# Optimization experiments

Hardware: AMD Instinct MI355X
Metric: run time of the kernel (lower is better)

The kernel has to match this reference:

```python
import jax, jax.numpy as jnp
import numpy as np


def _morpho(x, weight, bias, sign, padding, stride):
    # x: [B,C,H,W], weight: [B,C,kh,kw], bias: [B,C], sign: [B]
    B, C, H, W = x.shape
    kh, kw = weight.shape[-2:]
    # sign handling: if |sign| >= 1e-7 multiply by sign, else leave unchanged
    m = (jnp.abs(sign) >= 1e-7).astype(x.dtype)          # [B], constant (detached in torch)
    s = m * sign + (1.0 - m)                              # effective multiplier per sample
    xs = x * s[:, None, None, None]
    # unfold zero-pads, and sign*0 == 0, so padding signed x with zeros is equivalent
    xp = jnp.pad(xs, ((0, 0), (0, 0), (padding, padding), (padding, padding)))
    H2 = (H + 2 * padding - kh) // stride + 1
    W2 = (W + 2 * padding - kw) // stride + 1
    # direct windowed max-plus: y[b,c,i,j] = max_{p,q} xs_pad[b,c,i*s+p,j*s+q] + w[b,c,p,q]
    # small fixed kh*kw loop avoids materializing the B*C*kh*kw*L unfold tensor
    y = jnp.full((B, C, H2, W2), -jnp.inf, dtype=x.dtype)
    for p in range(kh):
        for q in range(kw):
            patch = jax.lax.slice(
                xp,
                (0, 0, p, q),
                (B, C, p + (H2 - 1) * stride + 1, q + (W2 - 1) * stride + 1),
                (1, 1, stride, stride),
            )  # [B,C,H2,W2]
            y = jnp.maximum(y, patch + weight[:, :, p, q][:, :, None, None])
    y = y + bias[:, :, None, None]
    return y * s[:, None, None, None]


def setup_inputs() -> dict:
    key = jax.random.key(0)
    k1, k2, k3, k4 = jax.random.split(key, 4)
    B, C, H, W, kh, kw = 16, 64, 128, 128, 5, 5
    return {
        "x": jax.random.normal(k1, (B, C, H, W), dtype=jnp.float32),
        "weight": jax.random.normal(k2, (B, C, kh, kw), dtype=jnp.float32) * 0.1,
        "bias": jax.random.normal(k3, (B, C), dtype=jnp.float32) * 0.1,
        "sign": jax.random.normal(k4, (B,), dtype=jnp.float32),
        "padding": 2,
        "stride": 1,
    }


def reference(x, weight, bias, sign, padding, stride):
    return _morpho(x, weight, bias, sign, padding, stride)
```

## Files before the change

### kernel.cpp

```cpp
#include <hip/hip_runtime.h>
#include <math.h>
#include <stdint.h>

#define HH 128
#define WW 128
#define LROWS 36
#define ROWU 72
#define UNITS 648
#define LDSU (LROWS * ROWU)

typedef __fp16 h2 __attribute__((ext_vector_type(2)));

__device__ __forceinline__ h2 h2max(h2 a, h2 b) { return __builtin_elementwise_max(a, b); }
__device__ __forceinline__ uint32_t h2u(h2 v) { return __builtin_bit_cast(uint32_t, v); }
__device__ __forceinline__ h2 uh2(uint32_t v) { return __builtin_bit_cast(h2, v); }

__global__ __launch_bounds__(256, 6) void morpho_kernel(
    const float* __restrict__ x,
    const float* __restrict__ wgt,
    const float* __restrict__ bias,
    const float* __restrict__ sign,
    float* __restrict__ out)
{
    __shared__ uint32_t lds[LDSU];

    const int blk  = blockIdx.x;
    const int quad = blk & 3;
    const int bc   = blk >> 2;
    const int b    = bc >> 6;

    const float* __restrict__ xp = x   + (size_t)bc * (HH * WW);
    float*       __restrict__ yp = out + (size_t)bc * (HH * WW);
    const float* __restrict__ wp = wgt + bc * 25;

    const float sgn = sign[b];
    const float s   = (fabsf(sgn) >= 1e-7f) ? sgn : 1.0f;
    const float bvs = bias[bc] * s;
    const __fp16 sh = (__fp16)s;
    const h2 s2 = { sh, sh };
    const h2 z2 = { (__fp16)0.f, (__fp16)0.f };

    const int t = threadIdx.x;

    float4 v0[3], v1[3];
    int urow[3], uuc[3];
    bool uin[3], uivalid[3];
#pragma unroll
    for (int k = 0; k < 3; ++k) {
        const int u   = t + k * 256;
        uin[k]        = (u < UNITS);
        const int row = u / 18;
        const int uc  = u - row * 18;
        urow[k] = row;  uuc[k] = uc;
        const int grow = quad * 32 - 2 + row;
        uivalid[k] = uin[k] && (uc >= 1) && (uc <= 16) && ((unsigned)grow < (unsigned)HH);
        const int rc = min(max(grow, 0), HH - 1);
        const int cc = min(max(uc * 8 - 8, 0), WW - 8);
        const float* gp = xp + rc * WW + cc;
        v0[k] = *reinterpret_cast<const float4*>(gp);
        v1[k] = *reinterpret_cast<const float4*>(gp + 4);
    }

    int ws[25];
#pragma unroll
    for (int k = 0; k < 25; ++k) {
        const __fp16 wh = (__fp16)wp[k];
        h2 wv2 = { wh, wh };
        ws[k] = __builtin_amdgcn_readfirstlane((int)h2u(wv2));
    }

#pragma unroll
    for (int k = 0; k < 3; ++k) {
        if (uin[k]) {
            const h2 m = uivalid[k] ? s2 : z2;
            const h2 h0 = __builtin_amdgcn_cvt_pkrtz(v0[k].x, v0[k].y) * m;
            const h2 h1 = __builtin_amdgcn_cvt_pkrtz(v0[k].z, v0[k].w) * m;
            const h2 hv = __builtin_amdgcn_cvt_pkrtz(v1[k].x, v1[k].y) * m;
            const h2 h3 = __builtin_amdgcn_cvt_pkrtz(v1[k].z, v1[k].w) * m;
            uint4 o;
            o.x = h2u(h0); o.y = h2u(h1); o.z = h2u(hv); o.w = h2u(h3);
            *reinterpret_cast<uint4*>(&lds[urow[k] * ROWU + uuc[k] * 4]) = o;
        }
    }

    __syncthreads();

    const int tx = t & 31;
    const int ty = t >> 5;
    h2 acc0[4], acc1[4];

#pragma unroll
    for (int r8 = 0; r8 < 8; ++r8) {
        const uint32_t* lp = &lds[(ty * 4 + r8) * ROWU + 2 * tx + 2];
        const uint32_t r1 = lp[1];
        const uint2   d23 = *reinterpret_cast<const uint2*>(lp + 2);
        const uint32_t r2 = d23.x, r3 = d23.y;
        const uint32_t r4 = lp[4];
        const uint32_t am1 = __builtin_amdgcn_alignbit(r2, r1, 16);
        const uint32_t a1  = __builtin_amdgcn_alignbit(r3, r2, 16);
        const uint32_t a3  = __builtin_amdgcn_alignbit(r4, r3, 16);
        const uint32_t P0a[5] = { r1, am1, r2, a1, r3 };
        const uint32_t P1a[5] = { r2, a1, r3, a3, r4 };

#pragma unroll
        for (int p = 0; p < 5; ++p) {
            const int oi = r8 - p;
            if (oi >= 0 && oi < 4) {
                {
                    const h2 t0 = uh2(P0a[0]) + uh2((uint32_t)ws[p * 5 + 0]);
                    const h2 t1 = uh2(P0a[1]) + uh2((uint32_t)ws[p * 5 + 1]);
                    const h2 t2 = uh2(P0a[2]) + uh2((uint32_t)ws[p * 5 + 2]);
                    const h2 t3 = uh2(P0a[3]) + uh2((uint32_t)ws[p * 5 + 3]);
                    const h2 t4 = uh2(P0a[4]) + uh2((uint32_t)ws[p * 5 + 4]);
                    h2 mm = h2max(h2max(h2max(t0, t1), h2max(t2, t3)), t4);
                    acc0[oi] = (p == 0) ? mm : h2max(acc0[oi], mm);
                }
                {
                    const h2 t0 = uh2(P1a[0]) + uh2((uint32_t)ws[p * 5 + 0]);
                    const h2 t1 = uh2(P1a[1]) + uh2((uint32_t)ws[p * 5 + 1]);
                    const h2 t2 = uh2(P1a[2]) + uh2((uint32_t)ws[p * 5 + 2]);
                    const h2 t3 = uh2(P1a[3]) + uh2((uint32_t)ws[p * 5 + 3]);
                    const h2 t4 = uh2(P1a[4]) + uh2((uint32_t)ws[p * 5 + 4]);
                    h2 mm = h2max(h2max(h2max(t0, t1), h2max(t2, t3)), t4);
                    acc1[oi] = (p == 0) ? mm : h2max(acc1[oi], mm);
                }
            }
        }
    }

    const int i0 = quad * 32 + ty * 4;
    const int j0 = tx * 4;
#pragma unroll
    for (int a = 0; a < 4; ++a) {
        float4 o;
        o.x = fmaf((float)acc0[a][0], s, bvs);
        o.y = fmaf((float)acc0[a][1], s, bvs);
        o.z = fmaf((float)acc1[a][0], s, bvs);
        o.w = fmaf((float)acc1[a][1], s, bvs);
        *reinterpret_cast<float4*>(yp + (size_t)(i0 + a) * WW + j0) = o;
    }
}

extern "C" void kernel_launch(void* const* d_in, const int* in_sizes, int n_in,
                              void* d_out, int out_size, void* d_ws, size_t ws_size,
                              hipStream_t stream) {
    (void)d_ws; (void)ws_size; (void)in_sizes; (void)n_in; (void)out_size;
    const float* x    = (const float*)d_in[0];
    const float* w    = (const float*)d_in[1];
    const float* bias = (const float*)d_in[2];
    const float* sign = (const float*)d_in[3];
    float* out = (float*)d_out;

    morpho_kernel<<<4096, 256, 0, stream>>>(x, w, bias, sign, out);
}
```

Before: 32.98 us.

## Replace LDS staging with direct global loads and fold sign into packed FMA

Drops the shared-memory tile and barrier. Each thread now loads its three float4 neighbours per input row straight from global memory and builds the shifted fp16 pairs in registers. The sign multiply moves from the staging step into a packed FMA with the weight. Block indices are remapped across the grid and launch bounds are raised to 8 waves per SIMD. This raises redundant global and L1/L2 traffic, since rows are reloaded by overlapping threads and blocks, in exchange for removing LDS writes and the sync and possibly raising occupancy.

```diff
diff --git a/kernel.cpp b/kernel.cpp
--- a/kernel.cpp
+++ b/kernel.cpp
@@ -4,10 +4,7 @@
 
 #define HH 128
 #define WW 128
-#define LROWS 36
-#define ROWU 72
-#define UNITS 648
-#define LDSU (LROWS * ROWU)
+#define NFLOATS (16 * 64 * HH * WW)
 
 typedef __fp16 h2 __attribute__((ext_vector_type(2)));
 
@@ -15,21 +12,25 @@
 __device__ __forceinline__ uint32_t h2u(h2 v) { return __builtin_bit_cast(uint32_t, v); }
 __device__ __forceinline__ h2 uh2(uint32_t v) { return __builtin_bit_cast(h2, v); }
 
-__global__ __launch_bounds__(256, 6) void morpho_kernel(
+#if __has_builtin(__builtin_elementwise_fma)
+#define H2FMA(a, b, c) __builtin_elementwise_fma((a), (b), (c))
+#else
+#define H2FMA(a, b, c) ((a) * (b) + (c))
+#endif
+
+__global__ __launch_bounds__(256, 8) void morpho_kernel(
     const float* __restrict__ x,
     const float* __restrict__ wgt,
     const float* __restrict__ bias,
     const float* __restrict__ sign,
     float* __restrict__ out)
 {
-    __shared__ uint32_t lds[LDSU];
-
-    const int blk  = blockIdx.x;
+    const int bid  = blockIdx.x;
+    const int blk  = (bid & 7) * 512 + (bid >> 3);
     const int quad = blk & 3;
     const int bc   = blk >> 2;
     const int b    = bc >> 6;
 
-    const float* __restrict__ xp = x   + (size_t)bc * (HH * WW);
     float*       __restrict__ yp = out + (size_t)bc * (HH * WW);
     const float* __restrict__ wp = wgt + bc * 25;
 
@@ -38,89 +39,78 @@
     const float bvs = bias[bc] * s;
     const __fp16 sh = (__fp16)s;
     const h2 s2 = { sh, sh };
-    const h2 z2 = { (__fp16)0.f, (__fp16)0.f };
 
-    const int t = threadIdx.x;
-
-    float4 v0[3], v1[3];
-    int urow[3], uuc[3];
-    bool uin[3], uivalid[3];
-#pragma unroll
-    for (int k = 0; k < 3; ++k) {
-        const int u   = t + k * 256;
-        uin[k]        = (u < UNITS);
-        const int row = u / 18;
-        const int uc  = u - row * 18;
-        urow[k] = row;  uuc[k] = uc;
-        const int grow = quad * 32 - 2 + row;
-        uivalid[k] = uin[k] && (uc >= 1) && (uc <= 16) && ((unsigned)grow < (unsigned)HH);
-        const int rc = min(max(grow, 0), HH - 1);
-        const int cc = min(max(uc * 8 - 8, 0), WW - 8);
-        const float* gp = xp + rc * WW + cc;
-        v0[k] = *reinterpret_cast<const float4*>(gp);
-        v1[k] = *reinterpret_cast<const float4*>(gp + 4);
-    }
-
-    int ws[25];
+    uint32_t wsu[25];
 #pragma unroll
     for (int k = 0; k < 25; ++k) {
         const __fp16 wh = (__fp16)wp[k];
-        h2 wv2 = { wh, wh };
-        ws[k] = __builtin_amdgcn_readfirstlane((int)h2u(wv2));
+        h2 w2 = { wh, wh };
+        wsu[k] = (uint32_t)__builtin_amdgcn_readfirstlane((int)h2u(w2));
     }
 
-#pragma unroll
-    for (int k = 0; k < 3; ++k) {
-        if (uin[k]) {
-            const h2 m = uivalid[k] ? s2 : z2;
-            const h2 h0 = __builtin_amdgcn_cvt_pkrtz(v0[k].x, v0[k].y) * m;
-            const h2 h1 = __builtin_amdgcn_cvt_pkrtz(v0[k].z, v0[k].w) * m;
-            const h2 hv = __builtin_amdgcn_cvt_pkrtz(v1[k].x, v1[k].y) * m;
-            const h2 h3 = __builtin_amdgcn_cvt_pkrtz(v1[k].z, v1[k].w) * m;
-            uint4 o;
-            o.x = h2u(h0); o.y = h2u(h1); o.z = h2u(hv); o.w = h2u(h3);
-            *reinterpret_cast<uint4*>(&lds[urow[k] * ROWU + uuc[k] * 4]) = o;
-        }
-    }
-
-    __syncthreads();
-
+    const int t  = threadIdx.x;
     const int tx = t & 31;
     const int ty = t >> 5;
+    const int j0 = tx * 4;
+    const int i0 = quad * 32 + ty * 4;
+    const int planeOff = bc * (HH * WW);
+
+    const bool mL = (tx > 0);
+    const bool mR = (tx < 31);
+
     h2 acc0[4], acc1[4];
 
 #pragma unroll
     for (int r8 = 0; r8 < 8; ++r8) {
-        const uint32_t* lp = &lds[(ty * 4 + r8) * ROWU + 2 * tx + 2];
-        const uint32_t r1 = lp[1];
-        const uint2   d23 = *reinterpret_cast<const uint2*>(lp + 2);
-        const uint32_t r2 = d23.x, r3 = d23.y;
-        const uint32_t r4 = lp[4];
-        const uint32_t am1 = __builtin_amdgcn_alignbit(r2, r1, 16);
-        const uint32_t a1  = __builtin_amdgcn_alignbit(r3, r2, 16);
-        const uint32_t a3  = __builtin_amdgcn_alignbit(r4, r3, 16);
-        const uint32_t P0a[5] = { r1, am1, r2, a1, r3 };
-        const uint32_t P1a[5] = { r2, a1, r3, a3, r4 };
+        const int  r  = i0 - 2 + r8;
+        const bool rv = ((unsigned)r < (unsigned)HH);
+        const int  rc = min(max(r, 0), HH - 1);
+        const int  oM = planeOff + rc * WW + j0;
+        const int  oL = max(oM - 4, 0);
+        const int  oR = min(oM + 4, NFLOATS - 4);
+        const float4 v0 = *reinterpret_cast<const float4*>(x + oL);
+        const float4 v1 = *reinterpret_cast<const float4*>(x + oM);
+        const float4 v2 = *reinterpret_cast<const float4*>(x + oR);
+
+        uint32_t e0 = h2u(__builtin_amdgcn_cvt_pkrtz(v0.z, v0.w));
+        uint32_t e1 = h2u(__builtin_amdgcn_cvt_pkrtz(v1.x, v1.y));
+        uint32_t e2 = h2u(__builtin_amdgcn_cvt_pkrtz(v1.z, v1.w));
+        uint32_t e3 = h2u(__builtin_amdgcn_cvt_pkrtz(v2.x, v2.y));
+        e0 = (rv && mL) ? e0 : 0u;
+        e1 = rv ? e1 : 0u;
+        e2 = rv ? e2 : 0u;
+        e3 = (rv && mR) ? e3 : 0u;
+        const uint32_t o0 = __builtin_amdgcn_alignbit(e1, e0, 16);
+        const uint32_t o1 = __builtin_amdgcn_alignbit(e2, e1, 16);
+        const uint32_t o2 = __builtin_amdgcn_alignbit(e3, e2, 16);
+
+        const uint32_t P0[5] = { e0, o0, e1, o1, e2 };
+        const uint32_t P1[5] = { e1, o1, e2, o2, e3 };
 
 #pragma unroll
         for (int p = 0; p < 5; ++p) {
             const int oi = r8 - p;
             if (oi >= 0 && oi < 4) {
+                const h2 w0 = uh2(wsu[p * 5 + 0]);
+                const h2 w1 = uh2(wsu[p * 5 + 1]);
+                const h2 w2 = uh2(wsu[p * 5 + 2]);
+                const h2 w3 = uh2(wsu[p * 5 + 3]);
+                const h2 w4 = uh2(wsu[p * 5 + 4]);
                 {
-                    const h2 t0 = uh2(P0a[0]) + uh2((uint32_t)ws[p * 5 + 0]);
-                    const h2 t1 = uh2(P0a[1]) + uh2((uint32_t)ws[p * 5 + 1]);
-                    const h2 t2 = uh2(P0a[2]) + uh2((uint32_t)ws[p * 5 + 2]);
-                    const h2 t3 = uh2(P0a[3]) + uh2((uint32_t)ws[p * 5 + 3]);
-                    const h2 t4 = uh2(P0a[4]) + uh2((uint32_t)ws[p * 5 + 4]);
+                    const h2 t0 = H2FMA(uh2(P0[0]), s2, w0);
+                    const h2 t1 = H2FMA(uh2(P0[1]), s2, w1);
+                    const h2 t2 = H2FMA(uh2(P0[2]), s2, w2);
+                    const h2 t3 = H2FMA(uh2(P0[3]), s2, w3);
+                    const h2 t4 = H2FMA(uh2(P0[4]), s2, w4);
                     h2 mm = h2max(h2max(h2max(t0, t1), h2max(t2, t3)), t4);
                     acc0[oi] = (p == 0) ? mm : h2max(acc0[oi], mm);
                 }
                 {
-                    const h2 t0 = uh2(P1a[0]) + uh2((uint32_t)ws[p * 5 + 0]);
-                    const h2 t1 = uh2(P1a[1]) + uh2((uint32_t)ws[p * 5 + 1]);
-                    const h2 t2 = uh2(P1a[2]) + uh2((uint32_t)ws[p * 5 + 2]);
-                    const h2 t3 = uh2(P1a[3]) + uh2((uint32_t)ws[p * 5 + 3]);
-                    const h2 t4 = uh2(P1a[4]) + uh2((uint32_t)ws[p * 5 + 4]);
+                    const h2 t0 = H2FMA(uh2(P1[0]), s2, w0);
+                    const h2 t1 = H2FMA(uh2(P1[1]), s2, w1);
+                    const h2 t2 = H2FMA(uh2(P1[2]), s2, w2);
+                    const h2 t3 = H2FMA(uh2(P1[3]), s2, w3);
+                    const h2 t4 = H2FMA(uh2(P1[4]), s2, w4);
                     h2 mm = h2max(h2max(h2max(t0, t1), h2max(t2, t3)), t4);
                     acc1[oi] = (p == 0) ? mm : h2max(acc1[oi], mm);
                 }
@@ -128,8 +118,6 @@
         }
     }
 
-    const int i0 = quad * 32 + ty * 4;
-    const int j0 = tx * 4;
 #pragma unroll
     for (int a = 0; a < 4; ++a) {
         float4 o;
```

Measured after the change: 33.54 us. No clear change (+1.7%).

## Process two row tiles per block with double-buffered LDS and up-front loads

Applied to the files above, without the earlier changes.

Each block now handles two 32-row tiles (half an image) instead of one. Global loads for both tiles are issued up front, and the second tile's conversion into a separate LDS buffer overlaps with the first tile's compute. The grid is halved and block IDs are remapped with an XCD-style swizzle. This amortizes the per-block weight setup and hides global latency, at the cost of doubled LDS and more registers, which can reduce occupancy under the existing launch bounds.

```diff
diff --git a/kernel.cpp b/kernel.cpp
--- a/kernel.cpp
+++ b/kernel.cpp
@@ -4,8 +4,8 @@
 
 #define HH 128
 #define WW 128
+#define ROWU 72
 #define LROWS 36
-#define ROWU 72
 #define UNITS 648
 #define LDSU (LROWS * ROWU)
 
@@ -22,11 +22,12 @@
     const float* __restrict__ sign,
     float* __restrict__ out)
 {
-    __shared__ uint32_t lds[LDSU];
+    __shared__ uint32_t lds[2][LDSU];
 
-    const int blk  = blockIdx.x;
-    const int quad = blk & 3;
-    const int bc   = blk >> 2;
+    const int bid  = blockIdx.x;
+    const int blk  = (bid & 7) * 256 + (bid >> 3);
+    const int half = blk & 1;
+    const int bc   = blk >> 1;
     const int b    = bc >> 6;
 
     const float* __restrict__ xp = x   + (size_t)bc * (HH * WW);
@@ -42,103 +43,125 @@
 
     const int t = threadIdx.x;
 
-    float4 v0[3], v1[3];
     int urow[3], uuc[3];
-    bool uin[3], uivalid[3];
+    bool uin[3];
 #pragma unroll
     for (int k = 0; k < 3; ++k) {
-        const int u   = t + k * 256;
-        uin[k]        = (u < UNITS);
-        const int row = u / 18;
-        const int uc  = u - row * 18;
-        urow[k] = row;  uuc[k] = uc;
-        const int grow = quad * 32 - 2 + row;
-        uivalid[k] = uin[k] && (uc >= 1) && (uc <= 16) && ((unsigned)grow < (unsigned)HH);
-        const int rc = min(max(grow, 0), HH - 1);
-        const int cc = min(max(uc * 8 - 8, 0), WW - 8);
-        const float* gp = xp + rc * WW + cc;
-        v0[k] = *reinterpret_cast<const float4*>(gp);
-        v1[k] = *reinterpret_cast<const float4*>(gp + 4);
+        const int u = t + k * 256;
+        uin[k] = (u < UNITS);
+        urow[k] = u / 18;
+        uuc[k]  = u - urow[k] * 18;
     }
 
-    int ws[25];
+    float4 vA0[3], vA1[3], vB0[3], vB1[3];
+#pragma unroll
+    for (int k = 0; k < 3; ++k) {
+        const int cc = min(max(uuc[k] * 8 - 8, 0), WW - 8);
+        {
+            const int grow = half * 64 - 2 + urow[k];
+            const int rc   = min(max(grow, 0), HH - 1);
+            const float* gp = xp + rc * WW + cc;
+            vA0[k] = *reinterpret_cast<const float4*>(gp);
+            vA1[k] = *reinterpret_cast<const float4*>(gp + 4);
+        }
+        {
+            const int grow = half * 64 + 30 + urow[k];
+            const int rc   = min(max(grow, 0), HH - 1);
+            const float* gp = xp + rc * WW + cc;
+            vB0[k] = *reinterpret_cast<const float4*>(gp);
+            vB1[k] = *reinterpret_cast<const float4*>(gp + 4);
+        }
+    }
+    asm volatile("" ::: "memory");
+
+    uint32_t wsu[25];
 #pragma unroll
     for (int k = 0; k < 25; ++k) {
         const __fp16 wh = (__fp16)wp[k];
-        h2 wv2 = { wh, wh };
-        ws[k] = __builtin_amdgcn_readfirstlane((int)h2u(wv2));
+        h2 w2 = { wh, wh };
+        wsu[k] = (uint32_t)__builtin_amdgcn_readfirstlane((int)h2u(w2));
     }
-
-#pragma unroll
-    for (int k = 0; k < 3; ++k) {
-        if (uin[k]) {
-            const h2 m = uivalid[k] ? s2 : z2;
-            const h2 h0 = __builtin_amdgcn_cvt_pkrtz(v0[k].x, v0[k].y) * m;
-            const h2 h1 = __builtin_amdgcn_cvt_pkrtz(v0[k].z, v0[k].w) * m;
-            const h2 hv = __builtin_amdgcn_cvt_pkrtz(v1[k].x, v1[k].y) * m;
-            const h2 h3 = __builtin_amdgcn_cvt_pkrtz(v1[k].z, v1[k].w) * m;
-            uint4 o;
-            o.x = h2u(h0); o.y = h2u(h1); o.z = h2u(hv); o.w = h2u(h3);
-            *reinterpret_cast<uint4*>(&lds[urow[k] * ROWU + uuc[k] * 4]) = o;
-        }
-    }
-
-    __syncthreads();
 
     const int tx = t & 31;
     const int ty = t >> 5;
-    h2 acc0[4], acc1[4];
+    const int j0 = tx * 4;
 
+    auto CVT_WRITE = [&](int buf, const float4* v0, const float4* v1, int tile) {
 #pragma unroll
-    for (int r8 = 0; r8 < 8; ++r8) {
-        const uint32_t* lp = &lds[(ty * 4 + r8) * ROWU + 2 * tx + 2];
-        const uint32_t r1 = lp[1];
-        const uint2   d23 = *reinterpret_cast<const uint2*>(lp + 2);
-        const uint32_t r2 = d23.x, r3 = d23.y;
-        const uint32_t r4 = lp[4];
-        const uint32_t am1 = __builtin_amdgcn_alignbit(r2, r1, 16);
-        const uint32_t a1  = __builtin_amdgcn_alignbit(r3, r2, 16);
-        const uint32_t a3  = __builtin_amdgcn_alignbit(r4, r3, 16);
-        const uint32_t P0a[5] = { r1, am1, r2, a1, r3 };
-        const uint32_t P1a[5] = { r2, a1, r3, a3, r4 };
+        for (int k = 0; k < 3; ++k) {
+            if (uin[k]) {
+                const int grow = half * 64 + tile * 32 - 2 + urow[k];
+                const bool valid = (uuc[k] >= 1) && (uuc[k] <= 16) &&
+                                   ((unsigned)grow < (unsigned)HH);
+                const h2 m = valid ? s2 : z2;
+                const h2 h0 = __builtin_amdgcn_cvt_pkrtz(v0[k].x, v0[k].y) * m;
+                const h2 h1 = __builtin_amdgcn_cvt_pkrtz(v0[k].z, v0[k].w) * m;
+                const h2 hv = __builtin_amdgcn_cvt_pkrtz(v1[k].x, v1[k].y) * m;
+                const h2 h3 = __builtin_amdgcn_cvt_pkrtz(v1[k].z, v1[k].w) * m;
+                uint4 o;
+                o.x = h2u(h0); o.y = h2u(h1); o.z = h2u(hv); o.w = h2u(h3);
+                *reinterpret_cast<uint4*>(&lds[buf][urow[k] * ROWU + uuc[k] * 4]) = o;
+            }
+        }
+    };
 
+    auto COMPUTE = [&](int buf, int tile) {
+        h2 acc0[4], acc1[4];
 #pragma unroll
-        for (int p = 0; p < 5; ++p) {
-            const int oi = r8 - p;
-            if (oi >= 0 && oi < 4) {
-                {
-                    const h2 t0 = uh2(P0a[0]) + uh2((uint32_t)ws[p * 5 + 0]);
-                    const h2 t1 = uh2(P0a[1]) + uh2((uint32_t)ws[p * 5 + 1]);
-                    const h2 t2 = uh2(P0a[2]) + uh2((uint32_t)ws[p * 5 + 2]);
-                    const h2 t3 = uh2(P0a[3]) + uh2((uint32_t)ws[p * 5 + 3]);
-                    const h2 t4 = uh2(P0a[4]) + uh2((uint32_t)ws[p * 5 + 4]);
-                    h2 mm = h2max(h2max(h2max(t0, t1), h2max(t2, t3)), t4);
-                    acc0[oi] = (p == 0) ? mm : h2max(acc0[oi], mm);
-                }
-                {
-                    const h2 t0 = uh2(P1a[0]) + uh2((uint32_t)ws[p * 5 + 0]);
-                    const h2 t1 = uh2(P1a[1]) + uh2((uint32_t)ws[p * 5 + 1]);
-                    const h2 t2 = uh2(P1a[2]) + uh2((uint32_t)ws[p * 5 + 2]);
-                    const h2 t3 = uh2(P1a[3]) + uh2((uint32_t)ws[p * 5 + 3]);
-                    const h2 t4 = uh2(P1a[4]) + uh2((uint32_t)ws[p * 5 + 4]);
-                    h2 mm = h2max(h2max(h2max(t0, t1), h2max(t2, t3)), t4);
-                    acc1[oi] = (p == 0) ? mm : h2max(acc1[oi], mm);
+        for (int r8 = 0; r8 < 8; ++r8) {
+            const uint32_t* lp = &lds[buf][(ty * 4 + r8) * ROWU + 2 * tx + 2];
+            const uint32_t r1 = lp[1];
+            const uint2  d23 = *reinterpret_cast<const uint2*>(lp + 2);
+            const uint32_t r2 = d23.x, r3 = d23.y;
+            const uint32_t r4 = lp[4];
+            const uint32_t o0 = __builtin_amdgcn_alignbit(r2, r1, 16);
+            const uint32_t o1 = __builtin_amdgcn_alignbit(r3, r2, 16);
+            const uint32_t o2 = __builtin_amdgcn_alignbit(r4, r3, 16);
+            const uint32_t P0[5] = { r1, o0, r2, o1, r3 };
+            const uint32_t P1[5] = { r2, o1, r3, o2, r4 };
+#pragma unroll
+            for (int p = 0; p < 5; ++p) {
+                const int oi = r8 - p;
+                if (oi >= 0 && oi < 4) {
+                    {
+                        const h2 t0 = uh2(P0[0]) + uh2(wsu[p * 5 + 0]);
+                        const h2 t1 = uh2(P0[1]) + uh2(wsu[p * 5 + 1]);
+                        const h2 t2 = uh2(P0[2]) + uh2(wsu[p * 5 + 2]);
+                        const h2 t3 = uh2(P0[3]) + uh2(wsu[p * 5 + 3]);
+                        const h2 t4 = uh2(P0[4]) + uh2(wsu[p * 5 + 4]);
+                        h2 mm = h2max(h2max(h2max(t0, t1), h2max(t2, t3)), t4);
+                        acc0[oi] = (p == 0) ? mm : h2max(acc0[oi], mm);
+                    }
+                    {
+                        const h2 t0 = uh2(P1[0]) + uh2(wsu[p * 5 + 0]);
+                        const h2 t1 = uh2(P1[1]) + uh2(wsu[p * 5 + 1]);
+                        const h2 t2 = uh2(P1[2]) + uh2(wsu[p * 5 + 2]);
+                        const h2 t3 = uh2(P1[3]) + uh2(wsu[p * 5 + 3]);
+                        const h2 t4 = uh2(P1[4]) + uh2(wsu[p * 5 + 4]);
+                        h2 mm = h2max(h2max(h2max(t0, t1), h2max(t2, t3)), t4);
+                        acc1[oi] = (p == 0) ? mm : h2max(acc1[oi], mm);
+                    }
                 }
             }
         }
-    }
+        const int i0 = half * 64 + tile * 32 + ty * 4;
+#pragma unroll
+        for (int a = 0; a < 4; ++a) {
+            float4 o;
+            o.x = fmaf((float)acc0[a][0], s, bvs);
+            o.y = fmaf((float)acc0[a][1], s, bvs);
+            o.z = fmaf((float)acc1[a][0], s, bvs);
+            o.w = fmaf((float)acc1[a][1], s, bvs);
+            *reinterpret_cast<float4*>(yp + (size_t)(i0 + a) * WW + j0) = o;
+        }
+    };
 
-    const int i0 = quad * 32 + ty * 4;
-    const int j0 = tx * 4;
-#pragma unroll
-    for (int a = 0; a < 4; ++a) {
-        float4 o;
-        o.x = fmaf((float)acc0[a][0], s, bvs);
-        o.y = fmaf((float)acc0[a][1], s, bvs);
-        o.z = fmaf((float)acc1[a][0], s, bvs);
-        o.w = fmaf((float)acc1[a][1], s, bvs);
-        *reinterpret_cast<float4*>(yp + (size_t)(i0 + a) * WW + j0) = o;
-    }
+    CVT_WRITE(0, vA0, vA1, 0);
+    __syncthreads();
+    COMPUTE(0, 0);
+    CVT_WRITE(1, vB0, vB1, 1);
+    __syncthreads();
+    COMPUTE(1, 1);
 }
 
 extern "C" void kernel_launch(void* const* d_in, const int* in_sizes, int n_in,
@@ -151,5 +174,5 @@
     const float* sign = (const float*)d_in[3];
     float* out = (float*)d_out;
 
-    morpho_kernel<<<4096, 256, 0, stream>>>(x, w, bias, sign, out);
+    morpho_kernel<<<2048, 256, 0, stream>>>(x, w, bias, sign, out);
 }
```

Result: no change. 33.25 us (+0.8%).
